# Kernel optimization log

Hardware: AMD Instinct MI355X
Metric: run time of the kernel (lower is better)

## Reference

```python
import jax, jax.numpy as jnp
import numpy as np
import math

N_HEAD = 8
HID_K = 128
HID_Q = 128


def setup_inputs() -> dict:
    key = jax.random.key(0)
    ks = jax.random.split(key, 6)
    B, KL, QL, EK, EQ = 32, 512, 512, 1024, 1024
    OUT = 1024
    return {
        "k": jax.random.normal(ks[0], (B, KL, EK), dtype=jnp.float32),
        "q": jax.random.normal(ks[1], (B, QL, EQ), dtype=jnp.float32),
        "w_kx": jax.random.normal(ks[2], (N_HEAD, EK, HID_K), dtype=jnp.float32) / math.sqrt(EK),
        "w_qx": jax.random.normal(ks[3], (N_HEAD, EQ, HID_Q), dtype=jnp.float32) / math.sqrt(EQ),
        "proj_w": jax.random.normal(ks[4], (OUT, N_HEAD * HID_K), dtype=jnp.float32) / math.sqrt(N_HEAD * HID_K),
        "proj_b": jnp.zeros((OUT,), dtype=jnp.float32),
    }


def reference(k, q, w_kx, w_qx, proj_w, proj_b):
    # k: (B, KL, EK), q: (B, QL, EQ)
    B, KL, _ = k.shape
    QL = q.shape[1]
    # per-head projections: (H, B, L, D)  -- matches torch repeat+bmm (head-major)
    kx = jnp.einsum("bke,hed->hbkd", k, w_kx)
    qx = jnp.einsum("bqe,hed->hbqd", q, w_qx)
    # scaled dot-product scores: (H, B, QL, KL)
    score = jnp.einsum("hbqd,hbkd->hbqk", qx, kx) / math.sqrt(HID_K)
    score = jax.nn.softmax(score, axis=-1)
    # context: (H, B, QL, D)
    ctx = jnp.einsum("hbqk,hbkd->hbqd", score, kx)
    # torch: split along head-major dim0 then cat on feature dim -> (B, QL, H*D)
    ctx = jnp.transpose(ctx, (1, 2, 0, 3)).reshape(B, QL, N_HEAD * HID_K)
    out = ctx @ proj_w.T + proj_b  # (B, QL, OUT); dropout=0 is identity
    # returned score matches torch shape (H*B, QL, KL), head-major
    return out, score.reshape(N_HEAD * B, QL, KL)
```

## Files before the change

kernel.cpp:

```cpp
#include <hip/hip_runtime.h>

typedef unsigned short u16;
typedef u16 u16x4 __attribute__((ext_vector_type(4)));
typedef u16 u16x8 __attribute__((ext_vector_type(8)));
typedef short bf16x8 __attribute__((ext_vector_type(8)));
typedef float f32x4 __attribute__((ext_vector_type(4)));

static __device__ __forceinline__ u16 f2bf(float f) {
  union { float f; unsigned u; } v; v.f = f;
  unsigned r = v.u + 0x7FFFu + ((v.u >> 16) & 1u);
  return (u16)(r >> 16);
}


template<bool A_F32, bool OUT_F32, bool WRITE_T, bool BIAS>
__global__ __launch_bounds__(256)
void gemm_bt(const void* __restrict__ A_, const u16* __restrict__ Bt,
             void* __restrict__ C_, u16* __restrict__ Ct,
             const float* __restrict__ bias,
             int M, int N, int K, int lda, int ldb, int ldc,
             long aSH, long aSB, long bSH, long bSB, long cSH, long cSB)
{
  constexpr int BM = 128, BN = 128, BK = 64, LDS_K = 72;
  __shared__ __align__(16) u16 As[BM][LDS_K];
  __shared__ __align__(16) u16 Bs[BN][LDS_K];

  const int tid  = threadIdx.x;
  const int lane = tid & 63;
  const int w    = tid >> 6;
  const int wr   = w >> 1, wc = w & 1;
  const int brow = blockIdx.y * BM;
  const int bcol = blockIdx.x * BN;
  const int zH = blockIdx.z >> 5, zB = blockIdx.z & 31;
  const long offA = (long)zH * aSH + (long)zB * aSB;
  const long offB = (long)zH * bSH + (long)zB * bSB;
  const long offC = (long)zH * cSH + (long)zB * cSB;
  const int kgrp = lane >> 4;
  const int l16  = lane & 15;

  f32x4 acc[4][4];
#pragma unroll
  for (int m = 0; m < 4; ++m)
#pragma unroll
    for (int n = 0; n < 4; ++n) acc[m][n] = f32x4{0.f, 0.f, 0.f, 0.f};

  for (int kt = 0; kt < K; kt += BK) {
    if constexpr (A_F32) {
      const float* A = (const float*)A_ + offA;
#pragma unroll
      for (int i = 0; i < 8; ++i) {
        int idx = i * 256 + tid;
        int row = idx >> 4, c4 = idx & 15;
        float4 v = *(const float4*)(A + (long)(brow + row) * lda + kt + c4 * 4);
        u16x4 b;
        b[0] = f2bf(v.x); b[1] = f2bf(v.y); b[2] = f2bf(v.z); b[3] = f2bf(v.w);
        *(u16x4*)(&As[row][c4 * 4]) = b;
      }
    } else {
      const u16* A = (const u16*)A_ + offA;
#pragma unroll
      for (int i = 0; i < 4; ++i) {
        int idx = i * 256 + tid;
        int row = idx >> 3, c8 = idx & 7;
        *(u16x8*)(&As[row][c8 * 8]) =
            *(const u16x8*)(A + (long)(brow + row) * lda + kt + c8 * 8);
      }
    }
#pragma unroll
    for (int i = 0; i < 4; ++i) {
      int idx = i * 256 + tid;
      int row = idx >> 3, c8 = idx & 7;
      *(u16x8*)(&Bs[row][c8 * 8]) =
          *(const u16x8*)(Bt + offB + (long)(bcol + row) * ldb + kt + c8 * 8);
    }
    __syncthreads();
#pragma unroll
    for (int kk = 0; kk < 2; ++kk) {
      bf16x8 af[4], bf[4];
#pragma unroll
      for (int m = 0; m < 4; ++m)
        af[m] = *(const bf16x8*)(&As[wr * 64 + m * 16 + l16][kk * 32 + kgrp * 8]);
#pragma unroll
      for (int n = 0; n < 4; ++n)
        bf[n] = *(const bf16x8*)(&Bs[wc * 64 + n * 16 + l16][kk * 32 + kgrp * 8]);
#pragma unroll
      for (int m = 0; m < 4; ++m)
#pragma unroll
        for (int n = 0; n < 4; ++n)
          acc[m][n] = __builtin_amdgcn_mfma_f32_16x16x32_bf16(af[m], bf[n], acc[m][n], 0, 0, 0);
    }
    __syncthreads();
  }

#pragma unroll
  for (int m = 0; m < 4; ++m) {
    const int gr0 = brow + wr * 64 + m * 16 + kgrp * 4;
#pragma unroll
    for (int n = 0; n < 4; ++n) {
      const int gc = bcol + wc * 64 + n * 16 + l16;
      if constexpr (OUT_F32) {
        float* C = (float*)C_ + offC;
        const float bv = BIAS ? bias[gc] : 0.0f;
#pragma unroll
        for (int j = 0; j < 4; ++j)
          C[(long)(gr0 + j) * ldc + gc] = acc[m][n][j] + bv;
      } else {
        u16* C = (u16*)C_ + offC;
#pragma unroll
        for (int j = 0; j < 4; ++j)
          C[(long)(gr0 + j) * ldc + gc] = f2bf(acc[m][n][j]);
        if constexpr (WRITE_T) {
          u16x4 t;
#pragma unroll
          for (int j = 0; j < 4; ++j) t[j] = f2bf(acc[m][n][j]);
          long ti = ((long)(gc >> 7) * 32 + (gr0 >> 9)) * 65536 + (long)(gc & 127) * 512 + (gr0 & 511);
          *(u16x4*)(Ct + ti) = t;
        }
      }
    }
  }
}

__global__ __launch_bounds__(256)
void attn_scores(const u16* __restrict__ qx, const u16* __restrict__ kx,
                 float* __restrict__ score)
{
  __shared__ __align__(16) u16 Ks[64][136];
  const int tid = threadIdx.x, lane = tid & 63, w = tid >> 6;
  const int bid = blockIdx.x;
  const int qt = bid & 7, hb = bid >> 3, h = hb >> 5, b = hb & 31;
  const int kgrp = lane >> 4, l16 = lane & 15;

  const u16* qrow = qx + ((long)(b * 512 + qt * 64 + w * 16 + l16)) * 1024 + h * 128 + kgrp * 8;
  bf16x8 qf[4];
#pragma unroll
  for (int kk = 0; kk < 4; ++kk) qf[kk] = *(const bf16x8*)(qrow + kk * 32);

  f32x4 acc[32];
#pragma unroll
  for (int n = 0; n < 32; ++n) acc[n] = f32x4{0.f, 0.f, 0.f, 0.f};

  const u16* kbase = kx + (long)b * 512 * 1024 + h * 128;
#pragma unroll
  for (int chunk = 0; chunk < 8; ++chunk) {
    __syncthreads();
#pragma unroll
    for (int i = 0; i < 4; ++i) {
      int idx = i * 256 + tid;
      int row = idx >> 4, c8 = idx & 15;
      *(u16x8*)(&Ks[row][c8 * 8]) =
          *(const u16x8*)(kbase + (long)(chunk * 64 + row) * 1024 + c8 * 8);
    }
    __syncthreads();
#pragma unroll
    for (int kk = 0; kk < 4; ++kk)
#pragma unroll
      for (int nl = 0; nl < 4; ++nl) {
        bf16x8 bf = *(const bf16x8*)(&Ks[nl * 16 + l16][kk * 32 + kgrp * 8]);
        acc[chunk * 4 + nl] =
            __builtin_amdgcn_mfma_f32_16x16x32_bf16(qf[kk], bf, acc[chunk * 4 + nl], 0, 0, 0);
      }
  }

  const float scale = 0.08838834764831845f;
#pragma unroll
  for (int j = 0; j < 4; ++j) {
    float m = -1e30f;
#pragma unroll
    for (int n = 0; n < 32; ++n) m = fmaxf(m, acc[n][j]);
    m = fmaxf(m, __shfl_xor(m, 1));
    m = fmaxf(m, __shfl_xor(m, 2));
    m = fmaxf(m, __shfl_xor(m, 4));
    m = fmaxf(m, __shfl_xor(m, 8));
    float s = 0.f;
#pragma unroll
    for (int n = 0; n < 32; ++n) {
      float e = __expf((acc[n][j] - m) * scale);
      acc[n][j] = e; s += e;
    }
    s += __shfl_xor(s, 1);
    s += __shfl_xor(s, 2);
    s += __shfl_xor(s, 4);
    s += __shfl_xor(s, 8);
    float inv = 1.0f / s;
#pragma unroll
    for (int n = 0; n < 32; ++n) acc[n][j] *= inv;
  }

  float* srow = score + ((long)hb * 512 + qt * 64 + w * 16 + kgrp * 4) * 512 + l16;
#pragma unroll
  for (int j = 0; j < 4; ++j)
#pragma unroll
    for (int n = 0; n < 32; ++n)
      srow[(long)j * 512 + n * 16] = acc[n][j];
}

__global__ __launch_bounds__(256)
void pack_whead(const float* __restrict__ w, u16* __restrict__ wT)
{
  long i = (long)blockIdx.x * 256 + threadIdx.x;
  int n = (int)(i >> 10), e = (int)(i & 1023);
  int h = n >> 7, d = n & 127;
  wT[i] = f2bf(w[((long)h * 1024 + e) * 128 + d]);
}

__global__ __launch_bounds__(256)
void pack_pw(const float4* __restrict__ w, u16x4* __restrict__ o)
{
  long i = (long)blockIdx.x * 256 + threadIdx.x;
  float4 v = w[i];
  u16x4 t;
  t[0] = f2bf(v.x); t[1] = f2bf(v.y); t[2] = f2bf(v.z); t[3] = f2bf(v.w);
  o[i] = t;
}

extern "C" void kernel_launch(void* const* d_in, const int* in_sizes, int n_in,
                              void* d_out, int out_size, void* d_ws, size_t ws_size,
                              hipStream_t stream)
{
  const float* k      = (const float*)d_in[0];
  const float* q      = (const float*)d_in[1];
  const float* w_kx   = (const float*)d_in[2];
  const float* w_qx   = (const float*)d_in[3];
  const float* proj_w = (const float*)d_in[4];
  const float* proj_b = (const float*)d_in[5];

  float* out   = (float*)d_out;
  float* score = (float*)d_out + 16777216;

  char* ws = (char*)d_ws;
  u16* wkT = (u16*)(ws + 0);
  u16* wqT = (u16*)(ws + (2l << 20));
  u16* pwB = (u16*)(ws + (4l << 20));
  u16* kx  = (u16*)(ws + (6l << 20));
  u16* qx  = (u16*)(ws + 39845888l);
  u16* kxT = (u16*)(ws + 73400320l);
  u16* ctx = (u16*)(ws + 106954752l);

  pack_whead<<<4096, 256, 0, stream>>>(w_kx, wkT);
  pack_whead<<<4096, 256, 0, stream>>>(w_qx, wqT);
  pack_pw<<<1024, 256, 0, stream>>>((const float4*)proj_w, (u16x4*)pwB);

  gemm_bt<true, false, true, false><<<dim3(8, 128, 1), 256, 0, stream>>>(
      k, wkT, kx, kxT, nullptr, 16384, 1024, 1024, 1024, 1024, 1024,
      0, 0, 0, 0, 0, 0);
  gemm_bt<true, false, false, false><<<dim3(8, 128, 1), 256, 0, stream>>>(
      q, wqT, qx, nullptr, nullptr, 16384, 1024, 1024, 1024, 1024, 1024,
      0, 0, 0, 0, 0, 0);

  attn_scores<<<2048, 256, 0, stream>>>(qx, kx, score);

  gemm_bt<true, false, false, false><<<dim3(1, 4, 256), 256, 0, stream>>>(
      score, kxT, ctx, nullptr, nullptr, 512, 128, 512, 512, 512, 1024,
      8388608l, 262144l, 2097152l, 65536l, 128l, 524288l);

  gemm_bt<false, true, false, true><<<dim3(8, 128, 1), 256, 0, stream>>>(
      ctx, pwB, out, nullptr, proj_b, 16384, 1024, 1024, 1024, 1024, 1024,
      0, 0, 0, 0, 0, 0);
}
```

Measured before the change: 800.7 us.

## Fuse softmax-times-V into score kernel and pre-convert inputs to bf16 with LDS DMA

The context matmul now happens inside the attention score kernel. Each wave writes its softmax probabilities as bf16 into LDS and multiplies them by kxT read straight from global memory, so the fp32 score matrix is no longer reloaded from HBM. The k and q inputs are converted to bf16 in separate pack kernels, and the projection GEMMs become a bf16-only kernel that loads tiles with global_load_lds direct-to-LDS transfers and an unpadded LDS layout. In exchange, the bf16 copies cost extra memory traffic, the unpadded layout may cause LDS bank conflicts, and the fused kernel's B operand comes from uncached global reads.

```diff
diff --git a/kernel.cpp b/kernel.cpp
--- a/kernel.cpp
+++ b/kernel.cpp
@@ -1,6 +1,7 @@
 #include <hip/hip_runtime.h>
 
 typedef unsigned short u16;
+typedef unsigned int u32;
 typedef u16 u16x4 __attribute__((ext_vector_type(4)));
 typedef u16 u16x8 __attribute__((ext_vector_type(8)));
 typedef short bf16x8 __attribute__((ext_vector_type(8)));
@@ -12,82 +13,64 @@
   return (u16)(r >> 16);
 }
 
-
-template<bool A_F32, bool OUT_F32, bool WRITE_T, bool BIAS>
-__global__ __launch_bounds__(256)
-void gemm_bt(const void* __restrict__ A_, const u16* __restrict__ Bt,
-             void* __restrict__ C_, u16* __restrict__ Ct,
-             const float* __restrict__ bias,
-             int M, int N, int K, int lda, int ldb, int ldc,
-             long aSH, long aSB, long bSH, long bSB, long cSH, long cSB)
-{
-  constexpr int BM = 128, BN = 128, BK = 64, LDS_K = 72;
-  __shared__ __align__(16) u16 As[BM][LDS_K];
-  __shared__ __align__(16) u16 Bs[BN][LDS_K];
+static __device__ __forceinline__ void gld_lds16(const u16* g, u16* l) {
+  __builtin_amdgcn_global_load_lds(
+      (const __attribute__((address_space(1))) u32*)g,
+      (__attribute__((address_space(3))) u32*)l, 16, 0, 0);
+}
+
+
+template<bool OUT_F32, bool WRITE_T, bool BIAS>
+__global__ __launch_bounds__(256)
+void gemm_bt16(const u16* __restrict__ A, const u16* __restrict__ Bt,
+               void* __restrict__ C_, u16* __restrict__ Ct,
+               const float* __restrict__ bias)
+{
+  constexpr int LD = 1024;
+  __shared__ __align__(16) u16 As[128 * 64];
+  __shared__ __align__(16) u16 Bs[128 * 64];
 
   const int tid  = threadIdx.x;
   const int lane = tid & 63;
   const int w    = tid >> 6;
   const int wr   = w >> 1, wc = w & 1;
-  const int brow = blockIdx.y * BM;
-  const int bcol = blockIdx.x * BN;
-  const int zH = blockIdx.z >> 5, zB = blockIdx.z & 31;
-  const long offA = (long)zH * aSH + (long)zB * aSB;
-  const long offB = (long)zH * bSH + (long)zB * bSB;
-  const long offC = (long)zH * cSH + (long)zB * cSB;
+  const int brow = blockIdx.y * 128;
+  const int bcol = blockIdx.x * 128;
   const int kgrp = lane >> 4;
   const int l16  = lane & 15;
 
+  const int srow = tid >> 3;
+  const int sc   = (tid & 7) * 8;
+
   f32x4 acc[4][4];
 #pragma unroll
   for (int m = 0; m < 4; ++m)
 #pragma unroll
     for (int n = 0; n < 4; ++n) acc[m][n] = f32x4{0.f, 0.f, 0.f, 0.f};
 
-  for (int kt = 0; kt < K; kt += BK) {
-    if constexpr (A_F32) {
-      const float* A = (const float*)A_ + offA;
-#pragma unroll
-      for (int i = 0; i < 8; ++i) {
-        int idx = i * 256 + tid;
-        int row = idx >> 4, c4 = idx & 15;
-        float4 v = *(const float4*)(A + (long)(brow + row) * lda + kt + c4 * 4);
-        u16x4 b;
-        b[0] = f2bf(v.x); b[1] = f2bf(v.y); b[2] = f2bf(v.z); b[3] = f2bf(v.w);
-        *(u16x4*)(&As[row][c4 * 4]) = b;
-      }
-    } else {
-      const u16* A = (const u16*)A_ + offA;
-#pragma unroll
-      for (int i = 0; i < 4; ++i) {
-        int idx = i * 256 + tid;
-        int row = idx >> 3, c8 = idx & 7;
-        *(u16x8*)(&As[row][c8 * 8]) =
-            *(const u16x8*)(A + (long)(brow + row) * lda + kt + c8 * 8);
-      }
-    }
+  for (int kt = 0; kt < 1024; kt += 64) {
+    const u16* Ab = A + (long)(brow + srow) * LD + kt + sc;
+    const u16* Bb = Bt + (long)(bcol + srow) * LD + kt + sc;
 #pragma unroll
     for (int i = 0; i < 4; ++i) {
-      int idx = i * 256 + tid;
-      int row = idx >> 3, c8 = idx & 7;
-      *(u16x8*)(&Bs[row][c8 * 8]) =
-          *(const u16x8*)(Bt + offB + (long)(bcol + row) * ldb + kt + c8 * 8);
+      gld_lds16(Ab + (long)i * 32 * LD, As + (i * 256 + tid) * 8);
+      gld_lds16(Bb + (long)i * 32 * LD, Bs + (i * 256 + tid) * 8);
     }
     __syncthreads();
 #pragma unroll
     for (int kk = 0; kk < 2; ++kk) {
-      bf16x8 af[4], bf[4];
+      bf16x8 af[4], bfr[4];
 #pragma unroll
       for (int m = 0; m < 4; ++m)
-        af[m] = *(const bf16x8*)(&As[wr * 64 + m * 16 + l16][kk * 32 + kgrp * 8]);
+        af[m] = *(const bf16x8*)(As + (wr * 64 + m * 16 + l16) * 64 + kk * 32 + kgrp * 8);
 #pragma unroll
       for (int n = 0; n < 4; ++n)
-        bf[n] = *(const bf16x8*)(&Bs[wc * 64 + n * 16 + l16][kk * 32 + kgrp * 8]);
+        bfr[n] = *(const bf16x8*)(Bs + (wc * 64 + n * 16 + l16) * 64 + kk * 32 + kgrp * 8);
 #pragma unroll
       for (int m = 0; m < 4; ++m)
 #pragma unroll
         for (int n = 0; n < 4; ++n)
-          acc[m][n] = __builtin_amdgcn_mfma_f32_16x16x32_bf16(af[m], bf[n], acc[m][n], 0, 0, 0);
+          acc[m][n] = __builtin_amdgcn_mfma_f32_16x16x32_bf16(af[m], bfr[n], acc[m][n], 0, 0, 0);
     }
     __syncthreads();
   }
@@ -99,16 +82,16 @@
     for (int n = 0; n < 4; ++n) {
       const int gc = bcol + wc * 64 + n * 16 + l16;
       if constexpr (OUT_F32) {
-        float* C = (float*)C_ + offC;
+        float* C = (float*)C_;
         const float bv = BIAS ? bias[gc] : 0.0f;
 #pragma unroll
         for (int j = 0; j < 4; ++j)
-          C[(long)(gr0 + j) * ldc + gc] = acc[m][n][j] + bv;
+          C[(long)(gr0 + j) * LD + gc] = acc[m][n][j] + bv;
       } else {
-        u16* C = (u16*)C_ + offC;
+        u16* C = (u16*)C_;
 #pragma unroll
         for (int j = 0; j < 4; ++j)
-          C[(long)(gr0 + j) * ldc + gc] = f2bf(acc[m][n][j]);
+          C[(long)(gr0 + j) * LD + gc] = f2bf(acc[m][n][j]);
         if constexpr (WRITE_T) {
           u16x4 t;
 #pragma unroll
@@ -122,10 +105,12 @@
 }
 
 __global__ __launch_bounds__(256)
-void attn_scores(const u16* __restrict__ qx, const u16* __restrict__ kx,
-                 float* __restrict__ score)
-{
-  __shared__ __align__(16) u16 Ks[64][136];
+void attn_fused(const u16* __restrict__ qx, const u16* __restrict__ kx,
+                const u16* __restrict__ kxT,
+                float* __restrict__ score, u16* __restrict__ ctx)
+{
+  __shared__ __align__(16) u16 lds[4 * 16 * 272];
+  u16 (*Ks)[136] = (u16(*)[136])lds;
   const int tid = threadIdx.x, lane = tid & 63, w = tid >> 6;
   const int bid = blockIdx.x;
   const int qt = bid & 7, hb = bid >> 3, h = hb >> 5, b = hb & 31;
@@ -141,7 +126,6 @@
   for (int n = 0; n < 32; ++n) acc[n] = f32x4{0.f, 0.f, 0.f, 0.f};
 
   const u16* kbase = kx + (long)b * 512 * 1024 + h * 128;
-#pragma unroll
   for (int chunk = 0; chunk < 8; ++chunk) {
     __syncthreads();
 #pragma unroll
@@ -156,9 +140,9 @@
     for (int kk = 0; kk < 4; ++kk)
 #pragma unroll
       for (int nl = 0; nl < 4; ++nl) {
-        bf16x8 bf = *(const bf16x8*)(&Ks[nl * 16 + l16][kk * 32 + kgrp * 8]);
+        bf16x8 bfr = *(const bf16x8*)(&Ks[nl * 16 + l16][kk * 32 + kgrp * 8]);
         acc[chunk * 4 + nl] =
-            __builtin_amdgcn_mfma_f32_16x16x32_bf16(qf[kk], bf, acc[chunk * 4 + nl], 0, 0, 0);
+            __builtin_amdgcn_mfma_f32_16x16x32_bf16(qf[kk], bfr, acc[chunk * 4 + nl], 0, 0, 0);
       }
   }
 
@@ -193,6 +177,49 @@
 #pragma unroll
     for (int n = 0; n < 32; ++n)
       srow[(long)j * 512 + n * 16] = acc[n][j];
+
+  u16* Pw = lds + w * 16 * 272;
+  f32x4 acc2[8];
+#pragma unroll
+  for (int n = 0; n < 8; ++n) acc2[n] = f32x4{0.f, 0.f, 0.f, 0.f};
+  const u16* kxTb = kxT + (long)hb * 65536;
+
+  for (int h2 = 0; h2 < 2; ++h2) {
+    __syncthreads();
+#pragma unroll
+    for (int j = 0; j < 4; ++j)
+#pragma unroll
+      for (int nn = 0; nn < 16; ++nn)
+        Pw[(kgrp * 4 + j) * 272 + l16 + nn * 16] = f2bf(acc[h2 * 16 + nn][j]);
+    __syncthreads();
+#pragma unroll
+    for (int ks = 0; ks < 8; ++ks) {
+      bf16x8 pa = *(const bf16x8*)(Pw + l16 * 272 + ks * 32 + kgrp * 8);
+      const u16* bbase = kxTb + (long)l16 * 512 + h2 * 256 + ks * 32 + kgrp * 8;
+#pragma unroll
+      for (int n = 0; n < 8; ++n) {
+        bf16x8 bb = *(const bf16x8*)(bbase + (long)n * 16 * 512);
+        acc2[n] = __builtin_amdgcn_mfma_f32_16x16x32_bf16(pa, bb, acc2[n], 0, 0, 0);
+      }
+    }
+  }
+
+  u16* crow = ctx + ((long)(b * 512 + qt * 64 + w * 16 + kgrp * 4)) * 1024 + h * 128 + l16;
+#pragma unroll
+  for (int n = 0; n < 8; ++n)
+#pragma unroll
+    for (int j = 0; j < 4; ++j)
+      crow[(long)j * 1024 + n * 16] = f2bf(acc2[n][j]);
+}
+
+__global__ __launch_bounds__(256)
+void pack_bf16(const float4* __restrict__ in, u16x4* __restrict__ o)
+{
+  long i = (long)blockIdx.x * 256 + threadIdx.x;
+  float4 v = in[i];
+  u16x4 t;
+  t[0] = f2bf(v.x); t[1] = f2bf(v.y); t[2] = f2bf(v.z); t[3] = f2bf(v.w);
+  o[i] = t;
 }
 
 __global__ __launch_bounds__(256)
@@ -202,16 +229,6 @@
   int n = (int)(i >> 10), e = (int)(i & 1023);
   int h = n >> 7, d = n & 127;
   wT[i] = f2bf(w[((long)h * 1024 + e) * 128 + d]);
-}
-
-__global__ __launch_bounds__(256)
-void pack_pw(const float4* __restrict__ w, u16x4* __restrict__ o)
-{
-  long i = (long)blockIdx.x * 256 + threadIdx.x;
-  float4 v = w[i];
-  u16x4 t;
-  t[0] = f2bf(v.x); t[1] = f2bf(v.y); t[2] = f2bf(v.z); t[3] = f2bf(v.w);
-  o[i] = t;
 }
 
 extern "C" void kernel_launch(void* const* d_in, const int* in_sizes, int n_in,
@@ -232,29 +249,23 @@
   u16* wkT = (u16*)(ws + 0);
   u16* wqT = (u16*)(ws + (2l << 20));
   u16* pwB = (u16*)(ws + (4l << 20));
-  u16* kx  = (u16*)(ws + (6l << 20));
-  u16* qx  = (u16*)(ws + 39845888l);
-  u16* kxT = (u16*)(ws + 73400320l);
-  u16* ctx = (u16*)(ws + 106954752l);
-
+  u16* kbf = (u16*)(ws + 6291456l);
+  u16* qbf = (u16*)(ws + 39845888l);
+  u16* kx  = (u16*)(ws + 73400320l);
+  u16* qx  = (u16*)(ws + 106954752l);
+  u16* kxT = (u16*)(ws + 140509184l);
+  u16* ctx = kbf;
+
+  pack_bf16<<<16384, 256, 0, stream>>>((const float4*)k, (u16x4*)kbf);
+  pack_bf16<<<16384, 256, 0, stream>>>((const float4*)q, (u16x4*)qbf);
+  pack_bf16<<<1024, 256, 0, stream>>>((const float4*)proj_w, (u16x4*)pwB);
   pack_whead<<<4096, 256, 0, stream>>>(w_kx, wkT);
   pack_whead<<<4096, 256, 0, stream>>>(w_qx, wqT);
-  pack_pw<<<1024, 256, 0, stream>>>((const float4*)proj_w, (u16x4*)pwB);
-
-  gemm_bt<true, false, true, false><<<dim3(8, 128, 1), 256, 0, stream>>>(
-      k, wkT, kx, kxT, nullptr, 16384, 1024, 1024, 1024, 1024, 1024,
-      0, 0, 0, 0, 0, 0);
-  gemm_bt<true, false, false, false><<<dim3(8, 128, 1), 256, 0, stream>>>(
-      q, wqT, qx, nullptr, nullptr, 16384, 1024, 1024, 1024, 1024, 1024,
-      0, 0, 0, 0, 0, 0);
-
-  attn_scores<<<2048, 256, 0, stream>>>(qx, kx, score);
-
-  gemm_bt<true, false, false, false><<<dim3(1, 4, 256), 256, 0, stream>>>(
-      score, kxT, ctx, nullptr, nullptr, 512, 128, 512, 512, 512, 1024,
-      8388608l, 262144l, 2097152l, 65536l, 128l, 524288l);
-
-  gemm_bt<false, true, false, true><<<dim3(8, 128, 1), 256, 0, stream>>>(
-      ctx, pwB, out, nullptr, proj_b, 16384, 1024, 1024, 1024, 1024, 1024,
-      0, 0, 0, 0, 0, 0);
-}
+
+  gemm_bt16<false, true, false><<<dim3(8, 128), 256, 0, stream>>>(kbf, wkT, kx, kxT, nullptr);
+  gemm_bt16<false, false, false><<<dim3(8, 128), 256, 0, stream>>>(qbf, wqT, qx, nullptr, nullptr);
+
+  attn_fused<<<2048, 256, 0, stream>>>(qx, kx, kxT, score, ctx);
+
+  gemm_bt16<true, false, true><<<dim3(8, 128), 256, 0, stream>>>(ctx, pwB, out, nullptr, proj_b);
+}
```

Result: slower. 881.2 us (+10.1%).
